# Optimization experiments

Measured on AMD Instinct MI355X. Metric: run time of the kernel, lower is better.

The kernel has to match this reference:

```python
import jax, jax.numpy as jnp
import numpy as np

N_NODES = 10000
N_EDGES = 80000
LATENT = 128
OUT_SIZE = 3
NODE_F = 12
EDGE_F = 7
STEPS = 15
LN_EPS = 1e-5


def _mlp(x, W0, b0, W1, b1, W2, b2):
    h = jax.nn.relu(x @ W0 + b0)
    h = jax.nn.relu(h @ W1 + b1)
    return h @ W2 + b2


def _ln(x, g, b):
    m = jnp.mean(x, axis=-1, keepdims=True)
    v = jnp.mean(jnp.square(x - m), axis=-1, keepdims=True)
    return (x - m) * jax.lax.rsqrt(v + LN_EPS) * g + b


def _forward(node_features, edge_features, senders, receivers,
             enW0, enb0, enW1, enb1, enW2, enb2, eng, enbe,
             eeW0, eeb0, eeW1, eeb1, eeW2, eeb2, eeg, eebe,
             beW0, beb0, beW1, beb1, beW2, beb2, beg, bebe,
             bnW0, bnb0, bnW1, bnb1, bnW2, bnb2, bng, bnbe,
             dW0, db0, dW1, db1, dW2, db2):
    # Encoder: node and mesh-edge MLPs with LayerNorm
    nl = _ln(_mlp(node_features, enW0, enb0, enW1, enb1, enW2, enb2), eng, enbe)  # [N, L]
    el = _ln(_mlp(edge_features, eeW0, eeb0, eeW1, eeb1, eeW2, eeb2), eeg, eebe)  # [E, L]

    # Processor: 15 GraphNetBlocks with residual connections, scanned over stacked params
    def block(carry, p):
        n, e = carry
        (eW0, eb0, eW1, eb1, eW2, eb2, eg, ebe,
         nW0, nb0, nW1, nb1, nW2, nb2, ng, nbe) = p
        feat = jnp.concatenate([n[senders], n[receivers], e], axis=-1)  # [E, 3L]
        new_e = _ln(_mlp(feat, eW0, eb0, eW1, eb1, eW2, eb2), eg, ebe)  # [E, L]
        agg = jax.ops.segment_sum(new_e, receivers, num_segments=N_NODES)  # [N, L]
        new_n = _ln(_mlp(jnp.concatenate([n, agg], axis=-1), nW0, nb0, nW1, nb1, nW2, nb2), ng, nbe)
        return (n + new_n, e + new_e), None

    xs = (beW0, beb0, beW1, beb1, beW2, beb2, beg, bebe,
          bnW0, bnb0, bnW1, bnb1, bnW2, bnb2, bng, bnbe)
    (nl, el), _ = jax.lax.scan(jax.checkpoint(block), (nl, el), xs)

    # Decoder: MLP without LayerNorm
    return _mlp(nl, dW0, db0, dW1, db1, dW2, db2)  # [N, OUT_SIZE]


def setup_inputs() -> dict:
    ks = iter(jax.random.split(jax.random.key(0), 32))

    def W(*shape):
        return jax.random.normal(next(ks), shape, jnp.float32) * (1.0 / np.sqrt(shape[-2]))

    z = lambda *s: jnp.zeros(s, jnp.float32)
    o = lambda *s: jnp.ones(s, jnp.float32)
    d = {}
    d['node_features'] = jax.random.normal(next(ks), (N_NODES, NODE_F), jnp.float32)
    d['edge_features'] = jax.random.normal(next(ks), (N_EDGES, EDGE_F), jnp.float32)
    d['senders'] = jax.random.randint(next(ks), (N_EDGES,), 0, N_NODES, jnp.int32)
    d['receivers'] = jax.random.randint(next(ks), (N_EDGES,), 0, N_NODES, jnp.int32)
    d.update(enW0=W(NODE_F, LATENT), enb0=z(LATENT), enW1=W(LATENT, LATENT), enb1=z(LATENT),
             enW2=W(LATENT, LATENT), enb2=z(LATENT), eng=o(LATENT), enbe=z(LATENT))
    d.update(eeW0=W(EDGE_F, LATENT), eeb0=z(LATENT), eeW1=W(LATENT, LATENT), eeb1=z(LATENT),
             eeW2=W(LATENT, LATENT), eeb2=z(LATENT), eeg=o(LATENT), eebe=z(LATENT))
    d.update(beW0=W(STEPS, 3 * LATENT, LATENT), beb0=z(STEPS, LATENT),
             beW1=W(STEPS, LATENT, LATENT), beb1=z(STEPS, LATENT),
             beW2=W(STEPS, LATENT, LATENT), beb2=z(STEPS, LATENT),
             beg=o(STEPS, LATENT), bebe=z(STEPS, LATENT))
    d.update(bnW0=W(STEPS, 2 * LATENT, LATENT), bnb0=z(STEPS, LATENT),
             bnW1=W(STEPS, LATENT, LATENT), bnb1=z(STEPS, LATENT),
             bnW2=W(STEPS, LATENT, LATENT), bnb2=z(STEPS, LATENT),
             bng=o(STEPS, LATENT), bnbe=z(STEPS, LATENT))
    d.update(dW0=W(LATENT, LATENT), db0=z(LATENT), dW1=W(LATENT, LATENT), db1=z(LATENT),
             dW2=W(LATENT, OUT_SIZE), db2=z(OUT_SIZE))
    return d


def reference(node_features, edge_features, senders, receivers,
              enW0, enb0, enW1, enb1, enW2, enb2, eng, enbe,
              eeW0, eeb0, eeW1, eeb1, eeW2, eeb2, eeg, eebe,
              beW0, beb0, beW1, beb1, beW2, beb2, beg, bebe,
              bnW0, bnb0, bnW1, bnb1, bnW2, bnb2, bng, bnbe,
              dW0, db0, dW1, db1, dW2, db2):
    return _forward(node_features, edge_features, senders, receivers,
                    enW0, enb0, enW1, enb1, enW2, enb2, eng, enbe,
                    eeW0, eeb0, eeW1, eeb1, eeW2, eeb2, eeg, eebe,
                    beW0, beb0, beW1, beb1, beW2, beb2, beg, bebe,
                    bnW0, bnb0, bnW1, bnb1, bnW2, bnb2, bng, bnbe,
                    dW0, db0, dW1, db1, dW2, db2)
```

## Files before the change

kernel.cpp:

```cpp
#include <hip/hip_runtime.h>
#include <hip/hip_bf16.h>
#include <stdint.h>

#define N_NODES 10000
#define N_EDGES 80000
#define L 128
#define STEPS 15
#define LN_EPS 1e-5f
#define NTHR 256
#define H_STRIDE 272

typedef short short8 __attribute__((ext_vector_type(8)));
typedef float floatx4 __attribute__((ext_vector_type(4)));

__device__ __forceinline__ float bf2f(const __hip_bfloat16 x) {
    return __bfloat162float(x);
}
__device__ __forceinline__ float ldmix(const void* p, int idx, int isf32) {
    return isf32 ? ((const float*)p)[idx]
                 : bf2f(((const __hip_bfloat16*)p)[idx]);
}

__global__ void detect_dtype(const uint32_t* __restrict__ nf, int* cnt) {
    int c = 0;
    for (int i = blockIdx.x * blockDim.x + threadIdx.x; i < 60000;
         i += gridDim.x * blockDim.x) {
        const uint32_t w = nf[i];
        c += (((w >> 7) & 0xFF) >= 0xC6) + (((w >> 23) & 0xFF) >= 0xC6);
    }
    atomicAdd(cnt, c);
}

#define N_TMATS 14
struct TAll {
    const void* src[N_TMATS];
    long long cum[N_TMATS + 1];
    int K[N_TMATS], N[N_TMATS], Kpad[N_TMATS];
};

__global__ void transpose_all(TAll a, const int* __restrict__ cnt,
                              __hip_bfloat16* __restrict__ pool) {
    const int isf32 = (*cnt > 1000);
    const long long total = a.cum[N_TMATS];
    for (long long i = blockIdx.x * (long long)blockDim.x + threadIdx.x;
         i < total; i += gridDim.x * (long long)blockDim.x) {
        int e = 0;
        #pragma unroll 1
        for (int j = 1; j < N_TMATS; j++) if (i >= a.cum[j]) e = j;
        const long long r = i - a.cum[e];
        const int per = a.N[e] * a.Kpad[e];
        const int m = (int)(r / per);
        int r2 = (int)(r - (long long)m * per);
        const int c2   = r2 >> 12;
        const int rem  = r2 & 4095;
        const int ct   = rem >> 9;
        const int lane = (rem >> 3) & 63;
        const int j    = rem & 7;
        const int k    = c2 * 32 + (lane >> 4) * 8 + j;
        const int col  = ct * 16 + (lane & 15);
        float v = 0.f;
        if (k < a.K[e]) v = ldmix(a.src[e], (m * a.K[e] + k) * a.N[e] + col, isf32);
        pool[i] = __float2bfloat16(v);
    }
}

__global__ void convert_feats(const void* __restrict__ nf,
                              const void* __restrict__ ef,
                              const int* __restrict__ cnt,
                              const int* __restrict__ elist,
                              __hip_bfloat16* __restrict__ fN,
                              __hip_bfloat16* __restrict__ fE)
{
    const int isf32 = (*cnt > 1000);
    const int totN = N_NODES * 32;
    const int totE = N_EDGES * 32;
    for (int i = blockIdx.x * blockDim.x + threadIdx.x; i < totN + totE;
         i += gridDim.x * blockDim.x) {
        if (i < totN) {
            const int r = i >> 5, c = i & 31;
            fN[i] = __float2bfloat16(c < 12 ? ldmix(nf, r * 12 + c, isf32) : 0.f);
        } else {
            const int j = i - totN;
            const int r = j >> 5, c = j & 31;
            const int e = elist[r];
            fE[j] = __float2bfloat16(c < 7 ? ldmix(ef, e * 7 + c, isf32) : 0.f);
        }
    }
}

__global__ void csr_hist(const int* __restrict__ rcv, int* __restrict__ deg) {
    for (int i = blockIdx.x * blockDim.x + threadIdx.x; i < N_EDGES;
         i += gridDim.x * blockDim.x)
        atomicAdd(&deg[rcv[i]], 1);
}

__global__ void csr_scan(const int* __restrict__ deg, int* __restrict__ rowptr,
                         int* __restrict__ cursor) {
    __shared__ int part[256];
    __shared__ int partx[257];
    const int t = threadIdx.x;
    int s = 0;
    for (int j = 0; j < 40; j++) {
        const int i = t * 40 + j;
        if (i < N_NODES) s += deg[i];
    }
    part[t] = s;
    __syncthreads();
    if (t == 0) {
        int r = 0;
        for (int k = 0; k < 256; k++) { partx[k] = r; r += part[k]; }
        partx[256] = r;
    }
    __syncthreads();
    int run = partx[t];
    for (int j = 0; j < 40; j++) {
        const int i = t * 40 + j;
        if (i < N_NODES) {
            rowptr[i] = run;
            cursor[i] = run;
            run += deg[i];
        }
    }
    if (t == 255) rowptr[N_NODES] = partx[256];
}

__global__ void csr_scatter(const int* __restrict__ rcv, int* __restrict__ cursor,
                            int* __restrict__ elist) {
    for (int i = blockIdx.x * blockDim.x + threadIdx.x; i < N_EDGES;
         i += gridDim.x * blockDim.x) {
        const int p = atomicAdd(&cursor[rcv[i]], 1);
        elist[p] = i;
    }
}

__global__ void sort_meta(const int* __restrict__ snd, const int* __restrict__ rcv,
                          const int* __restrict__ elist,
                          int* __restrict__ ssnd, int* __restrict__ srcv) {
    for (int i = blockIdx.x * blockDim.x + threadIdx.x; i < N_EDGES;
         i += gridDim.x * blockDim.x) {
        const int e = elist[i];
        ssnd[i] = snd[e];
        srcv[i] = rcv[e];
    }
}

__global__ __launch_bounds__(256)
void csr_agg(const int* __restrict__ rowptr,
             const __hip_bfloat16* __restrict__ ln16,
             __hip_bfloat16* __restrict__ agg16)
{
    const int g = threadIdx.x >> 5;
    const int lane = threadIdx.x & 31;
    const int v = blockIdx.x * 8 + g;
    if (v >= N_NODES) return;
    const int c0 = lane * 4;
    float s0 = 0.f, s1 = 0.f, s2 = 0.f, s3 = 0.f;
    int j = rowptr[v];
    const int en = rowptr[v + 1];
    for (; j + 1 < en; j += 2) {
        union { uint2 w; __hip_bfloat16 h[4]; } u0, u1;
        u0.w = *(const uint2*)(ln16 + (size_t)j * L + c0);
        u1.w = *(const uint2*)(ln16 + (size_t)(j + 1) * L + c0);
        s0 += bf2f(u0.h[0]); s1 += bf2f(u0.h[1]); s2 += bf2f(u0.h[2]); s3 += bf2f(u0.h[3]);
        s0 += bf2f(u1.h[0]); s1 += bf2f(u1.h[1]); s2 += bf2f(u1.h[2]); s3 += bf2f(u1.h[3]);
    }
    for (; j < en; j++) {
        union { uint2 w; __hip_bfloat16 h[4]; } u;
        u.w = *(const uint2*)(ln16 + (size_t)j * L + c0);
        s0 += bf2f(u.h[0]); s1 += bf2f(u.h[1]); s2 += bf2f(u.h[2]); s3 += bf2f(u.h[3]);
    }
    union { uint2 w; __hip_bfloat16 h[4]; } o;
    o.h[0] = __float2bfloat16(s0); o.h[1] = __float2bfloat16(s1);
    o.h[2] = __float2bfloat16(s2); o.h[3] = __float2bfloat16(s3);
    *(uint2*)(agg16 + (size_t)v * L + c0) = o.w;
}

enum AMode { A_PLAIN = 0, A_FEAT = 1, A_CAT = 2 };
enum Epi   { E_LN_STORE = 0, E_LN_EDGE = 1, E_LN_NODE = 2, E_DEC = 3 };

template <int AMODE, int EPI, int NL, int K0>
__global__ __launch_bounds__(NTHR, 4)
void fused_mlp(const __hip_bfloat16* __restrict__ A, int lda, int M,
               const __hip_bfloat16* __restrict__ WT0,
               const __hip_bfloat16* __restrict__ WT1,
               const __hip_bfloat16* __restrict__ WT2,
               const void* __restrict__ b0,
               const void* __restrict__ b1,
               const void* __restrict__ b2,
               const void* __restrict__ g,
               const void* __restrict__ beta,
               int poff,
               const int* __restrict__ cnt,
               const __hip_bfloat16* __restrict__ n16,
               const __hip_bfloat16* __restrict__ e16s,
               const __hip_bfloat16* __restrict__ agg16,
               const int* __restrict__ ssnd,
               const int* __restrict__ srcv,
               float* res32,
               __hip_bfloat16* res16,
               __hip_bfloat16* __restrict__ lnout,
               const void* __restrict__ dW,
               const void* __restrict__ db,
               void* __restrict__ dout)
{
    __shared__ __align__(16) char lds[17408 + 16384];
    char* wbuf = lds + 17408;

    const int tid  = threadIdx.x;
    const int wv   = tid >> 6;
    const int lane = tid & 63;
    const int quad = lane >> 4;
    const int m15  = lane & 15;
    const int row0 = blockIdx.x * 64;
    const int isf32 = (*cnt > 1000);

    char* hw = lds + wv * 4352;

    const int rw = row0 + wv * 16 + m15;
    const int rc = rw < M ? rw : M - 1;

    int sI = 0, rI = 0;
    if constexpr (AMODE == A_FEAT) { sI = ssnd[rc]; rI = srcv[rc]; }

    auto aFrag = [&](int kchunk) -> short8 {
        const int k0 = kchunk * 32 + quad * 8;
        const __hip_bfloat16* sp;
        if constexpr (AMODE == A_PLAIN) {
            sp = A + (size_t)rc * lda + k0;
        } else if constexpr (AMODE == A_FEAT) {
            if (k0 < L)          sp = n16  + (size_t)sI * L + k0;
            else if (k0 < 2 * L) sp = n16  + (size_t)rI * L + (k0 - L);
            else                 sp = e16s + (size_t)rc * L + (k0 - 2 * L);
        } else {
            if (k0 < L) sp = n16   + (size_t)rc * L + k0;
            else        sp = agg16 + (size_t)rc * L + (k0 - L);
        }
        return *(const short8*)sp;
    };
    auto loadWc = [&](const __hip_bfloat16* base, int c, int4& x, int4& y) {
        const __hip_bfloat16* p = base + (size_t)c * 4096 + tid * 16;
        x = *(const int4*)p;
        y = *(const int4*)(p + 8);
    };
    auto storeWc = [&](int b, const int4& x, const int4& y) {
        *(int4*)(wbuf + b * 8192 + tid * 32)      = x;
        *(int4*)(wbuf + b * 8192 + tid * 32 + 16) = y;
    };
    auto breadc = [&](int b, int ct) -> short8 {
        return *(const short8*)(wbuf + b * 8192 + ct * 1024 + lane * 16);
    };

    constexpr int C0 = K0 / 32;

    int4 w0, w1;
    short8 aCur, aNext;
    int buf = 0;
    floatx4 acc[8];

    #pragma unroll
    for (int ct = 0; ct < 8; ct++) acc[ct] = (floatx4)0.f;

    loadWc(WT0, 0, w0, w1);
    aCur = aFrag(0);
    if constexpr (C0 > 1) aNext = aFrag(1);

    for (int c = 0; c < C0; c++) {
        storeWc(buf, w0, w1);
        __syncthreads();
        const short8 a = aCur;
        aCur = aNext;
        if (c + 2 < C0) aNext = aFrag(c + 2);
        if (c + 1 < C0) loadWc(WT0, c + 1, w0, w1);
        else            loadWc(WT1, 0, w0, w1);
        #pragma unroll
        for (int ct = 0; ct < 8; ct++)
            acc[ct] = __builtin_amdgcn_mfma_f32_16x16x32_bf16(a, breadc(buf, ct), acc[ct], 0, 0, 0);
        buf ^= 1;
    }
    {
        float bb[8];
        #pragma unroll
        for (int ct = 0; ct < 8; ct++) bb[ct] = ldmix(b0, poff + ct * 16 + m15, isf32);
        #pragma unroll
        for (int ct = 0; ct < 8; ct++)
            #pragma unroll
            for (int i = 0; i < 4; i++) {
                const int rl = quad * 4 + i;
                const int col = ct * 16 + m15;
                *(__hip_bfloat16*)(hw + rl * H_STRIDE + col * 2) =
                    __float2bfloat16(fmaxf(acc[ct][i] + bb[ct], 0.f));
            }
    }

    {
        #pragma unroll
        for (int ct = 0; ct < 8; ct++) acc[ct] = (floatx4)0.f;
        short8 af[4];
        #pragma unroll
        for (int c = 0; c < 4; c++)
            af[c] = *(const short8*)(hw + m15 * H_STRIDE + c * 64 + quad * 16);
        for (int c = 0; c < 4; c++) {
            storeWc(buf, w0, w1);
            __syncthreads();
            if (c < 3)               loadWc(WT1, c + 1, w0, w1);
            else if constexpr (NL == 3) loadWc(WT2, 0, w0, w1);
            #pragma unroll
            for (int ct = 0; ct < 8; ct++)
                acc[ct] = __builtin_amdgcn_mfma_f32_16x16x32_bf16(af[c], breadc(buf, ct), acc[ct], 0, 0, 0);
            buf ^= 1;
        }
        float bb[8];
        #pragma unroll
        for (int ct = 0; ct < 8; ct++) bb[ct] = ldmix(b1, poff + ct * 16 + m15, isf32);
        #pragma unroll
        for (int ct = 0; ct < 8; ct++)
            #pragma unroll
            for (int i = 0; i < 4; i++) {
                const int rl = quad * 4 + i;
                const int col = ct * 16 + m15;
                *(__hip_bfloat16*)(hw + rl * H_STRIDE + col * 2) =
                    __float2bfloat16(fmaxf(acc[ct][i] + bb[ct], 0.f));
            }
    }

    if constexpr (NL == 3) {
        #pragma unroll
        for (int ct = 0; ct < 8; ct++) acc[ct] = (floatx4)0.f;
        short8 af[4];
        #pragma unroll
        for (int c = 0; c < 4; c++)
            af[c] = *(const short8*)(hw + m15 * H_STRIDE + c * 64 + quad * 16);
        for (int c = 0; c < 4; c++) {
            storeWc(buf, w0, w1);
            __syncthreads();
            if (c < 3) loadWc(WT2, c + 1, w0, w1);
            #pragma unroll
            for (int ct = 0; ct < 8; ct++)
                acc[ct] = __builtin_amdgcn_mfma_f32_16x16x32_bf16(af[c], breadc(buf, ct), acc[ct], 0, 0, 0);
            buf ^= 1;
        }
        float bb[8], gg[8], be[8];
        #pragma unroll
        for (int ct = 0; ct < 8; ct++) {
            bb[ct] = ldmix(b2,   poff + ct * 16 + m15, isf32);
            gg[ct] = ldmix(g,    poff + ct * 16 + m15, isf32);
            be[ct] = ldmix(beta, poff + ct * 16 + m15, isf32);
        }
        #pragma unroll
        for (int i = 0; i < 4; i++) {
            float t[8], s = 0.f, s2 = 0.f;
            #pragma unroll
            for (int ct = 0; ct < 8; ct++) {
                t[ct] = acc[ct][i] + bb[ct];
                s  += t[ct];
                s2 += t[ct] * t[ct];
            }
            #pragma unroll
            for (int m = 1; m < 16; m <<= 1) {
                s  += __shfl_xor(s,  m, 64);
                s2 += __shfl_xor(s2, m, 64);
            }
            const float mean = s * (1.f / 128.f);
            const float var  = s2 * (1.f / 128.f) - mean * mean;
            const float inv  = rsqrtf(fmaxf(var, 0.f) + LN_EPS);
            const int rg = row0 + wv * 16 + quad * 4 + i;
            if (rg < M) {
                #pragma unroll
                for (int ct = 0; ct < 8; ct++) {
                    const int col = ct * 16 + m15;
                    const float o = (t[ct] - mean) * inv * gg[ct] + be[ct];
                    const size_t idx = (size_t)rg * L + col;
                    if constexpr (EPI == E_LN_STORE) {
                        res32[idx] = o;
                        if (res16) res16[idx] = __float2bfloat16(o);
                    } else if constexpr (EPI == E_LN_NODE) {
                        const float nw = res32[idx] + o;
                        res32[idx] = nw;
                        res16[idx] = __float2bfloat16(nw);
                    } else {
                        const float nw = res32[idx] + o;
                        res32[idx] = nw;
                        res16[idx] = __float2bfloat16(nw);
                        lnout[idx] = __float2bfloat16(o);
                    }
                }
            }
        }
    } else {
        __syncthreads();
        float* Wl = (float*)wbuf;
        for (int i = tid; i < 3 * L; i += NTHR) {
            const int o = i / L, k = i - o * L;
            Wl[o * L + k] = ldmix(dW, k * 3 + o, isf32);
        }
        __syncthreads();
        if (tid < 64) {
            const int rg = row0 + tid;
            if (rg < M) {
                const __hip_bfloat16* hr =
                    (const __hip_bfloat16*)(lds + (tid >> 4) * 4352 + (tid & 15) * H_STRIDE);
                float s0 = ldmix(db, 0, isf32);
                float s1 = ldmix(db, 1, isf32);
                float s2 = ldmix(db, 2, isf32);
                #pragma unroll 8
                for (int k = 0; k < L; k++) {
                    const float hv = bf2f(hr[k]);
                    s0 += hv * Wl[k];
                    s1 += hv * Wl[L + k];
                    s2 += hv * Wl[2 * L + k];
                }
                if (isf32) {
                    float* o = (float*)dout;
                    o[rg * 3 + 0] = s0; o[rg * 3 + 1] = s1; o[rg * 3 + 2] = s2;
                } else {
                    __hip_bfloat16* o = (__hip_bfloat16*)dout;
                    o[rg * 3 + 0] = __float2bfloat16(s0);
                    o[rg * 3 + 1] = __float2bfloat16(s1);
                    o[rg * 3 + 2] = __float2bfloat16(s2);
                }
            }
        }
    }
}

extern "C" void kernel_launch(void* const* d_in, const int* in_sizes, int n_in,
                              void* d_out, int out_size, void* d_ws, size_t ws_size,
                              hipStream_t stream)
{
    (void)in_sizes; (void)n_in; (void)out_size; (void)ws_size;
    const int* snd = (const int*)d_in[2];
    const int* rcv = (const int*)d_in[3];

    char* ws = (char*)d_ws;
    int* cnt = (int*)ws;                              ws += 256;
    auto takeB = [&](size_t el) {
        __hip_bfloat16* p = (__hip_bfloat16*)ws;
        ws += ((el * 2 + 255) & ~255ull);
        return p;
    };
    auto takeF = [&](size_t el) {
        float* p = (float*)ws;
        ws += ((el * 4 + 255) & ~255ull);
        return p;
    };
    auto takeI = [&](size_t el) {
        int* p = (int*)ws;
        ws += ((el * 4 + 255) & ~255ull);
        return p;
    };

    const int srcIdx[N_TMATS] = {4, 6, 8, 12, 14, 16, 20, 22, 24, 28, 30, 32, 36, 38};
    const int tK[N_TMATS]    = {12, 128, 128, 7, 128, 128, 384, 128, 128, 256, 128, 128, 128, 128};
    const int tKp[N_TMATS]   = {32, 128, 128, 32, 128, 128, 384, 128, 128, 256, 128, 128, 128, 128};
    const int tNm[N_TMATS]   = {1, 1, 1, 1, 1, 1, STEPS, STEPS, STEPS, STEPS, STEPS, STEPS, 1, 1};
    TAll ta;
    long long cum = 0;
    __hip_bfloat16* wmat[N_TMATS];
    __hip_bfloat16* wpool = (__hip_bfloat16*)ws;
    for (int j = 0; j < N_TMATS; j++) {
        ta.src[j] = d_in[srcIdx[j]];
        ta.cum[j] = cum;
        ta.K[j] = tK[j]; ta.N[j] = 128; ta.Kpad[j] = tKp[j];
        wmat[j] = wpool + cum;
        cum += (long long)tNm[j] * 128 * tKp[j];
    }
    ta.cum[N_TMATS] = cum;
    ws += ((cum * 2 + 255) & ~255ull);

    float* n32 = takeF((size_t)N_NODES * L);
    float* e32 = takeF((size_t)N_EDGES * L);
    __hip_bfloat16* n16   = takeB((size_t)N_NODES * L);
    __hip_bfloat16* e16   = takeB((size_t)N_EDGES * L);
    __hip_bfloat16* ln16  = takeB((size_t)N_EDGES * L);
    __hip_bfloat16* agg16 = takeB((size_t)N_NODES * L);
    __hip_bfloat16* fN16  = takeB((size_t)N_NODES * 32);
    __hip_bfloat16* fE16  = takeB((size_t)N_EDGES * 32);
    int* deg    = takeI(N_NODES);
    int* rowptr = takeI(N_NODES + 1);
    int* cursor = takeI(N_NODES);
    int* elist  = takeI(N_EDGES);
    int* ssnd   = takeI(N_EDGES);
    int* srcv   = takeI(N_EDGES);

    const dim3 blk(NTHR);
    const dim3 grdE((N_EDGES + 63) / 64);
    const dim3 grdN((N_NODES + 63) / 64);

    (void)hipMemsetAsync(cnt, 0, sizeof(int), stream);
    (void)hipMemsetAsync(deg, 0, N_NODES * sizeof(int), stream);
    detect_dtype<<<dim3(64), blk, 0, stream>>>((const uint32_t*)d_in[0], cnt);
    transpose_all<<<dim3(512), blk, 0, stream>>>(ta, cnt, wpool);

    csr_hist<<<dim3(80), blk, 0, stream>>>(rcv, deg);
    csr_scan<<<dim3(1), blk, 0, stream>>>(deg, rowptr, cursor);
    csr_scatter<<<dim3(80), blk, 0, stream>>>(rcv, cursor, elist);
    sort_meta<<<dim3(80), blk, 0, stream>>>(snd, rcv, elist, ssnd, srcv);
    convert_feats<<<dim3(256), blk, 0, stream>>>(d_in[0], d_in[1], cnt, elist, fN16, fE16);

    fused_mlp<A_PLAIN, E_LN_STORE, 3, 32><<<grdE, blk, 0, stream>>>(
        fE16, 32, N_EDGES, wmat[3], wmat[4], wmat[5],
        d_in[13], d_in[15], d_in[17], d_in[18], d_in[19], 0, cnt,
        nullptr, nullptr, nullptr, nullptr, nullptr,
        e32, e16, nullptr, nullptr, nullptr, nullptr);
    fused_mlp<A_PLAIN, E_LN_STORE, 3, 32><<<grdN, blk, 0, stream>>>(
        fN16, 32, N_NODES, wmat[0], wmat[1], wmat[2],
        d_in[5], d_in[7], d_in[9], d_in[10], d_in[11], 0, cnt,
        nullptr, nullptr, nullptr, nullptr, nullptr,
        n32, n16, nullptr, nullptr, nullptr, nullptr);

    for (int s = 0; s < STEPS; s++) {
        const int po = s * L;
        fused_mlp<A_FEAT, E_LN_EDGE, 3, 384><<<grdE, blk, 0, stream>>>(
            nullptr, 0, N_EDGES,
            wmat[6] + (size_t)s * 128 * 384,
            wmat[7] + (size_t)s * 128 * 128,
            wmat[8] + (size_t)s * 128 * 128,
            d_in[21], d_in[23], d_in[25], d_in[26], d_in[27], po, cnt,
            n16, e16, nullptr, ssnd, srcv,
            e32, e16, ln16, nullptr, nullptr, nullptr);
        csr_agg<<<dim3((N_NODES + 7) / 8), blk, 0, stream>>>(rowptr, ln16, agg16);
        fused_mlp<A_CAT, E_LN_NODE, 3, 256><<<grdN, blk, 0, stream>>>(
            nullptr, 0, N_NODES,
            wmat[9]  + (size_t)s * 128 * 256,
            wmat[10] + (size_t)s * 128 * 128,
            wmat[11] + (size_t)s * 128 * 128,
            d_in[29], d_in[31], d_in[33], d_in[34], d_in[35], po, cnt,
            n16, nullptr, agg16, nullptr, nullptr,
            n32, n16, nullptr, nullptr, nullptr, nullptr);
    }

    fused_mlp<A_PLAIN, E_DEC, 2, 128><<<grdN, blk, 0, stream>>>(
        n16, 128, N_NODES, wmat[12], wmat[13], nullptr,
        d_in[37], d_in[39], nullptr, nullptr, nullptr, 0, cnt,
        nullptr, nullptr, nullptr, nullptr, nullptr,
        nullptr, nullptr, nullptr, d_in[40], d_in[41], d_out);
}
```

Baseline: 1.464 ms.

## Stage A and weight tiles through padded LDS with plain row-major weight layout

Replaces the pre-swizzled MFMA-fragment weight layout with a plain transposed [N][Kpad] layout and loads both A and weight tiles cooperatively into padded (80-byte stride) LDS buffers each 32-wide K chunk. It also remaps block indices in groups of eight and turns K0 into a runtime argument. The intent is coalesced cooperative A loads, particularly for the gathered edge features, instead of per-lane fragment gathers. In exchange it adds an extra barrier per chunk, single-buffers the weights, and drops the prefetch across layers. K0 becoming runtime may also limit unrolling.

```diff
diff --git a/kernel.cpp b/kernel.cpp
--- a/kernel.cpp
+++ b/kernel.cpp
@@ -50,16 +50,11 @@
         const long long r = i - a.cum[e];
         const int per = a.N[e] * a.Kpad[e];
         const int m = (int)(r / per);
-        int r2 = (int)(r - (long long)m * per);
-        const int c2   = r2 >> 12;
-        const int rem  = r2 & 4095;
-        const int ct   = rem >> 9;
-        const int lane = (rem >> 3) & 63;
-        const int j    = rem & 7;
-        const int k    = c2 * 32 + (lane >> 4) * 8 + j;
-        const int col  = ct * 16 + (lane & 15);
+        const int r2 = (int)(r - (long long)m * per);
+        const int nn = r2 / a.Kpad[e];
+        const int kk = r2 - nn * a.Kpad[e];
         float v = 0.f;
-        if (k < a.K[e]) v = ldmix(a.src[e], (m * a.K[e] + k) * a.N[e] + col, isf32);
+        if (kk < a.K[e]) v = ldmix(a.src[e], (m * a.K[e] + kk) * a.N[e] + nn, isf32);
         pool[i] = __float2bfloat16(v);
     }
 }
@@ -178,9 +173,9 @@
 enum AMode { A_PLAIN = 0, A_FEAT = 1, A_CAT = 2 };
 enum Epi   { E_LN_STORE = 0, E_LN_EDGE = 1, E_LN_NODE = 2, E_DEC = 3 };
 
-template <int AMODE, int EPI, int NL, int K0>
+template <int AMODE, int EPI, int NL>
 __global__ __launch_bounds__(NTHR, 4)
-void fused_mlp(const __hip_bfloat16* __restrict__ A, int lda, int M,
+void fused_mlp(const __hip_bfloat16* __restrict__ A, int lda, int M, int K0,
                const __hip_bfloat16* __restrict__ WT0,
                const __hip_bfloat16* __restrict__ WT1,
                const __hip_bfloat16* __restrict__ WT2,
@@ -203,79 +198,97 @@
                const void* __restrict__ db,
                void* __restrict__ dout)
 {
-    __shared__ __align__(16) char lds[17408 + 16384];
-    char* wbuf = lds + 17408;
+    __shared__ __align__(16) char lds[17408 + 10240];
+    char* AsB = lds;
+    char* WsB = lds + 17408;
+
+    const int nb  = gridDim.x;
+    const int per = nb >> 3;
+    const int bid = blockIdx.x;
+    int sb = bid;
+    if (bid < per * 8) sb = (bid & 7) * per + (bid >> 3);
 
     const int tid  = threadIdx.x;
     const int wv   = tid >> 6;
     const int lane = tid & 63;
     const int quad = lane >> 4;
     const int m15  = lane & 15;
-    const int row0 = blockIdx.x * 64;
+    const int row0 = sb * 64;
     const int isf32 = (*cnt > 1000);
 
     char* hw = lds + wv * 4352;
 
-    const int rw = row0 + wv * 16 + m15;
-    const int rc = rw < M ? rw : M - 1;
-
-    int sI = 0, rI = 0;
-    if constexpr (AMODE == A_FEAT) { sI = ssnd[rc]; rI = srcv[rc]; }
-
-    auto aFrag = [&](int kchunk) -> short8 {
-        const int k0 = kchunk * 32 + quad * 8;
-        const __hip_bfloat16* sp;
-        if constexpr (AMODE == A_PLAIN) {
-            sp = A + (size_t)rc * lda + k0;
-        } else if constexpr (AMODE == A_FEAT) {
-            if (k0 < L)          sp = n16  + (size_t)sI * L + k0;
-            else if (k0 < 2 * L) sp = n16  + (size_t)rI * L + (k0 - L);
-            else                 sp = e16s + (size_t)rc * L + (k0 - 2 * L);
-        } else {
-            if (k0 < L) sp = n16   + (size_t)rc * L + k0;
-            else        sp = agg16 + (size_t)rc * L + (k0 - L);
-        }
-        return *(const short8*)sp;
+    const int boff = m15 * 80 + quad * 16;
+    const int aoff = (wv * 16 + m15) * 80 + quad * 16;
+
+    const int aq   = tid & 3;
+    const int arow = tid >> 2;
+    int sidx = 0, ridx = 0;
+    {
+        const int rg = row0 + arow;
+        if constexpr (AMODE == A_FEAT) {
+            sidx = (rg < M) ? ssnd[rg] : 0;
+            ridx = (rg < M) ? srcv[rg] : 0;
+        }
+    }
+
+    auto loadA = [&](int k0) -> int4 {
+        const int rg = row0 + arow;
+        int4 av = make_int4(0, 0, 0, 0);
+        if (rg < M) {
+            if constexpr (AMODE == A_PLAIN) {
+                av = *(const int4*)(A + (size_t)rg * lda + k0 + aq * 8);
+            } else if constexpr (AMODE == A_FEAT) {
+                const __hip_bfloat16* sp;
+                if (k0 < 2 * L) {
+                    const int nd = (k0 < L) ? sidx : ridx;
+                    sp = n16 + (size_t)nd * L + (k0 & (L - 1)) + aq * 8;
+                } else {
+                    sp = e16s + (size_t)rg * L + (k0 - 2 * L) + aq * 8;
+                }
+                av = *(const int4*)sp;
+            } else {
+                const __hip_bfloat16* sp = (k0 < L)
+                    ? n16   + (size_t)rg * L + k0 + aq * 8
+                    : agg16 + (size_t)rg * L + (k0 - L) + aq * 8;
+                av = *(const int4*)sp;
+            }
+        }
+        return av;
     };
-    auto loadWc = [&](const __hip_bfloat16* base, int c, int4& x, int4& y) {
-        const __hip_bfloat16* p = base + (size_t)c * 4096 + tid * 16;
-        x = *(const int4*)p;
-        y = *(const int4*)(p + 8);
+    auto loadW = [&](const __hip_bfloat16* WT, int ksz, int k0) -> int4 {
+        return *(const int4*)(WT + (size_t)(tid >> 2) * ksz + k0 + aq * 8);
     };
-    auto storeWc = [&](int b, const int4& x, const int4& y) {
-        *(int4*)(wbuf + b * 8192 + tid * 32)      = x;
-        *(int4*)(wbuf + b * 8192 + tid * 32 + 16) = y;
+    auto loadW2 = [&](const __hip_bfloat16* WT, int ksz, int k0) -> int4 {
+        return *(const int4*)(WT + (size_t)((tid >> 2) + 64) * ksz + k0 + aq * 8);
     };
-    auto breadc = [&](int b, int ct) -> short8 {
-        return *(const short8*)(wbuf + b * 8192 + ct * 1024 + lane * 16);
-    };
-
-    constexpr int C0 = K0 / 32;
-
-    int4 w0, w1;
-    short8 aCur, aNext;
-    int buf = 0;
+
     floatx4 acc[8];
 
     #pragma unroll
     for (int ct = 0; ct < 8; ct++) acc[ct] = (floatx4)0.f;
 
-    loadWc(WT0, 0, w0, w1);
-    aCur = aFrag(0);
-    if constexpr (C0 > 1) aNext = aFrag(1);
-
-    for (int c = 0; c < C0; c++) {
-        storeWc(buf, w0, w1);
+    int4 pA = loadA(0);
+    int4 pW0 = loadW(WT0, K0, 0);
+    int4 pW1 = loadW2(WT0, K0, 0);
+
+    for (int k0 = 0; k0 < K0; k0 += 32) {
+        *(int4*)(AsB + arow * 80 + aq * 16) = pA;
+        *(int4*)(WsB + arow * 80 + aq * 16)        = pW0;
+        *(int4*)(WsB + (arow + 64) * 80 + aq * 16) = pW1;
         __syncthreads();
-        const short8 a = aCur;
-        aCur = aNext;
-        if (c + 2 < C0) aNext = aFrag(c + 2);
-        if (c + 1 < C0) loadWc(WT0, c + 1, w0, w1);
-        else            loadWc(WT1, 0, w0, w1);
-        #pragma unroll
-        for (int ct = 0; ct < 8; ct++)
-            acc[ct] = __builtin_amdgcn_mfma_f32_16x16x32_bf16(a, breadc(buf, ct), acc[ct], 0, 0, 0);
-        buf ^= 1;
+        if (k0 + 32 < K0) {
+            pA  = loadA(k0 + 32);
+            pW0 = loadW(WT0, K0, k0 + 32);
+            pW1 = loadW2(WT0, K0, k0 + 32);
+        }
+        const short8 a = *(const short8*)(AsB + aoff);
+        #pragma unroll
+        for (int ct = 0; ct < 8; ct++) {
+            const short8 b = *(const short8*)(WsB + boff + ct * 1280);
+            acc[ct] = __builtin_amdgcn_mfma_f32_16x16x32_bf16(a, b, acc[ct], 0, 0, 0);
+        }
+        __syncthreads();
     }
     {
         float bb[8];
@@ -299,15 +312,22 @@
         #pragma unroll
         for (int c = 0; c < 4; c++)
             af[c] = *(const short8*)(hw + m15 * H_STRIDE + c * 64 + quad * 16);
+        int4 qW0 = loadW(WT1, L, 0);
+        int4 qW1 = loadW2(WT1, L, 0);
         for (int c = 0; c < 4; c++) {
-            storeWc(buf, w0, w1);
+            *(int4*)(WsB + arow * 80 + aq * 16)        = qW0;
+            *(int4*)(WsB + (arow + 64) * 80 + aq * 16) = qW1;
             __syncthreads();
-            if (c < 3)               loadWc(WT1, c + 1, w0, w1);
-            else if constexpr (NL == 3) loadWc(WT2, 0, w0, w1);
+            if (c < 3) {
+                qW0 = loadW(WT1, L, (c + 1) * 32);
+                qW1 = loadW2(WT1, L, (c + 1) * 32);
+            }
             #pragma unroll
-            for (int ct = 0; ct < 8; ct++)
-                acc[ct] = __builtin_amdgcn_mfma_f32_16x16x32_bf16(af[c], breadc(buf, ct), acc[ct], 0, 0, 0);
-            buf ^= 1;
+            for (int ct = 0; ct < 8; ct++) {
+                const short8 b = *(const short8*)(WsB + boff + ct * 1280);
+                acc[ct] = __builtin_amdgcn_mfma_f32_16x16x32_bf16(af[c], b, acc[ct], 0, 0, 0);
+            }
+            __syncthreads();
         }
         float bb[8];
         #pragma unroll
@@ -330,14 +350,22 @@
         #pragma unroll
         for (int c = 0; c < 4; c++)
             af[c] = *(const short8*)(hw + m15 * H_STRIDE + c * 64 + quad * 16);
+        int4 qW0 = loadW(WT2, L, 0);
+        int4 qW1 = loadW2(WT2, L, 0);
         for (int c = 0; c < 4; c++) {
-            storeWc(buf, w0, w1);
+            *(int4*)(WsB + arow * 80 + aq * 16)        = qW0;
+            *(int4*)(WsB + (arow + 64) * 80 + aq * 16) = qW1;
             __syncthreads();
-            if (c < 3) loadWc(WT2, c + 1, w0, w1);
+            if (c < 3) {
+                qW0 = loadW(WT2, L, (c + 1) * 32);
+                qW1 = loadW2(WT2, L, (c + 1) * 32);
+            }
             #pragma unroll
-            for (int ct = 0; ct < 8; ct++)
-                acc[ct] = __builtin_amdgcn_mfma_f32_16x16x32_bf16(af[c], breadc(buf, ct), acc[ct], 0, 0, 0);
-            buf ^= 1;
+            for (int ct = 0; ct < 8; ct++) {
+                const short8 b = *(const short8*)(WsB + boff + ct * 1280);
+                acc[ct] = __builtin_amdgcn_mfma_f32_16x16x32_bf16(af[c], b, acc[ct], 0, 0, 0);
+            }
+            __syncthreads();
         }
         float bb[8], gg[8], be[8];
         #pragma unroll
@@ -388,7 +416,7 @@
         }
     } else {
         __syncthreads();
-        float* Wl = (float*)wbuf;
+        float* Wl = (float*)WsB;
         for (int i = tid; i < 3 * L; i += NTHR) {
             const int o = i / L, k = i - o * L;
             Wl[o * L + k] = ldmix(dW, k * 3 + o, isf32);
@@ -497,21 +525,21 @@
     sort_meta<<<dim3(80), blk, 0, stream>>>(snd, rcv, elist, ssnd, srcv);
     convert_feats<<<dim3(256), blk, 0, stream>>>(d_in[0], d_in[1], cnt, elist, fN16, fE16);
 
-    fused_mlp<A_PLAIN, E_LN_STORE, 3, 32><<<grdE, blk, 0, stream>>>(
-        fE16, 32, N_EDGES, wmat[3], wmat[4], wmat[5],
+    fused_mlp<A_PLAIN, E_LN_STORE, 3><<<grdE, blk, 0, stream>>>(
+        fE16, 32, N_EDGES, 32, wmat[3], wmat[4], wmat[5],
         d_in[13], d_in[15], d_in[17], d_in[18], d_in[19], 0, cnt,
         nullptr, nullptr, nullptr, nullptr, nullptr,
         e32, e16, nullptr, nullptr, nullptr, nullptr);
-    fused_mlp<A_PLAIN, E_LN_STORE, 3, 32><<<grdN, blk, 0, stream>>>(
-        fN16, 32, N_NODES, wmat[0], wmat[1], wmat[2],
+    fused_mlp<A_PLAIN, E_LN_STORE, 3><<<grdN, blk, 0, stream>>>(
+        fN16, 32, N_NODES, 32, wmat[0], wmat[1], wmat[2],
         d_in[5], d_in[7], d_in[9], d_in[10], d_in[11], 0, cnt,
         nullptr, nullptr, nullptr, nullptr, nullptr,
         n32, n16, nullptr, nullptr, nullptr, nullptr);
 
     for (int s = 0; s < STEPS; s++) {
         const int po = s * L;
-        fused_mlp<A_FEAT, E_LN_EDGE, 3, 384><<<grdE, blk, 0, stream>>>(
-            nullptr, 0, N_EDGES,
+        fused_mlp<A_FEAT, E_LN_EDGE, 3><<<grdE, blk, 0, stream>>>(
+            nullptr, 0, N_EDGES, 384,
             wmat[6] + (size_t)s * 128 * 384,
             wmat[7] + (size_t)s * 128 * 128,
             wmat[8] + (size_t)s * 128 * 128,
@@ -519,8 +547,8 @@
             n16, e16, nullptr, ssnd, srcv,
             e32, e16, ln16, nullptr, nullptr, nullptr);
         csr_agg<<<dim3((N_NODES + 7) / 8), blk, 0, stream>>>(rowptr, ln16, agg16);
-        fused_mlp<A_CAT, E_LN_NODE, 3, 256><<<grdN, blk, 0, stream>>>(
-            nullptr, 0, N_NODES,
+        fused_mlp<A_CAT, E_LN_NODE, 3><<<grdN, blk, 0, stream>>>(
+            nullptr, 0, N_NODES, 256,
             wmat[9]  + (size_t)s * 128 * 256,
             wmat[10] + (size_t)s * 128 * 128,
             wmat[11] + (size_t)s * 128 * 128,
@@ -529,8 +557,8 @@
             n32, n16, nullptr, nullptr, nullptr, nullptr);
     }
 
-    fused_mlp<A_PLAIN, E_DEC, 2, 128><<<grdN, blk, 0, stream>>>(
-        n16, 128, N_NODES, wmat[12], wmat[13], nullptr,
+    fused_mlp<A_PLAIN, E_DEC, 2><<<grdN, blk, 0, stream>>>(
+        n16, 128, N_NODES, 128, wmat[12], wmat[13], nullptr,
         d_in[37], d_in[39], nullptr, nullptr, nullptr, 0, cnt,
         nullptr, nullptr, nullptr, nullptr, nullptr,
         nullptr, nullptr, nullptr, d_in[40], d_in[41], d_out);
```

Result: faster. 1.320 ms (-9.8%).
